# Performance work log

Measured on AMD Instinct MI355X. Metric: run time of the kernel, lower is better.

## Reference

```python
import jax, jax.numpy as jnp
from jax import lax
import numpy as np

IMG = 1024
STRIDES = (4, 8, 16, 32, 64)
FEAT_HW = (256, 128, 64, 32, 16)
ANCHOR_SCALE = 8.0          # per-level scale multiplier of stride
RATIOS = (0.5, 1.0, 2.0)
N_ANCHOR = len(RATIOS)
PRE_NMS = 6000
POST_NMS = 300
NMS_THRESH = 0.7
MIN_SIZE = 16.0
IMG_SCALE = 1.0
NEG = -1e9


def _conv(x, w, b, pad):
    y = lax.conv_general_dilated(x, w, (1, 1), [(pad, pad), (pad, pad)],
                                 dimension_numbers=("NCHW", "OIHW", "NCHW"))
    return y + b[None, :, None, None]


def _level_anchors(H, W, stride):
    # base anchors (ymin,xmin,ymax,xmax) centered at 0, one scale per level
    r = jnp.asarray(RATIOS, jnp.float32)
    hs = stride * ANCHOR_SCALE * jnp.sqrt(r)
    ws = stride * ANCHOR_SCALE * jnp.sqrt(1.0 / r)
    base = jnp.stack([-hs / 2, -ws / 2, hs / 2, ws / 2], axis=1)  # [A,4]
    ys = jnp.arange(H, dtype=jnp.float32) * stride
    xs = jnp.arange(W, dtype=jnp.float32) * stride
    gy, gx = jnp.meshgrid(ys, xs, indexing="ij")
    shift = jnp.stack([gy, gx, gy, gx], axis=-1).reshape(-1, 1, 4)   # [HW,1,4]
    return (shift + base[None, :, :]).reshape(-1, 4)                 # [HW*A,4]


def _decode(anchors, loc):
    ah = anchors[:, 2] - anchors[:, 0]
    aw = anchors[:, 3] - anchors[:, 1]
    acy = anchors[:, 0] + 0.5 * ah
    acx = anchors[:, 1] + 0.5 * aw
    dy, dx, dh, dw = loc[:, 0], loc[:, 1], loc[:, 2], loc[:, 3]
    cy = dy * ah + acy
    cx = dx * aw + acx
    h = jnp.exp(dh) * ah
    w = jnp.exp(dw) * aw
    boxes = jnp.stack([cy - 0.5 * h, cx - 0.5 * w, cy + 0.5 * h, cx + 0.5 * w], axis=1)
    return jnp.clip(boxes, 0.0, float(IMG))


def _iou_row(box, boxes):
    ty = jnp.maximum(box[0], boxes[:, 0])
    tx = jnp.maximum(box[1], boxes[:, 1])
    by = jnp.minimum(box[2], boxes[:, 2])
    bx = jnp.minimum(box[3], boxes[:, 3])
    inter = jnp.maximum(by - ty, 0.0) * jnp.maximum(bx - tx, 0.0)
    a1 = (box[2] - box[0]) * (box[3] - box[1])
    a2 = (boxes[:, 2] - boxes[:, 0]) * (boxes[:, 3] - boxes[:, 1])
    return inter / jnp.maximum(a1 + a2 - inter, 1e-9)


def _nms(boxes, scores):
    n = boxes.shape[0]
    idx_range = jnp.arange(n)

    def body(sc, _):
        i = jnp.argmax(sc)
        valid = sc[i] > NEG / 2
        iou = _iou_row(boxes[i], boxes)
        new_sc = jnp.where((iou > NMS_THRESH) | (idx_range == i), NEG, sc)
        sc = jnp.where(valid, new_sc, sc)
        return sc, (i, valid)

    _, (idx, keep) = lax.scan(body, scores, None, length=POST_NMS)
    return boxes[idx] * keep[:, None].astype(boxes.dtype)


def reference(p2, p3, p4, p5, p6, conv_w, conv_b, loc_w, loc_b, score_w, score_b):
    feats = [p2, p3, p4, p5, p6]
    locs, fgs, anchors = [], [], []
    for f, stride in zip(feats, STRIDES):
        h = jax.nn.relu(_conv(f, conv_w, conv_b, 1))
        loc = _conv(h, loc_w, loc_b, 0)        # [1,4A,H,W]
        sc = _conv(h, score_w, score_b, 0)     # [1,2A,H,W]
        H, W = loc.shape[2], loc.shape[3]
        loc = loc.transpose(0, 2, 3, 1).reshape(-1, 4)          # [HWA,4]
        sc = sc.transpose(0, 2, 3, 1).reshape(-1, 2)            # [HWA,2]
        fgs.append(jax.nn.softmax(sc, axis=-1)[:, 1])
        locs.append(loc)
        anchors.append(_level_anchors(H, W, stride))
    loc = jnp.concatenate(locs, axis=0)
    fg = jnp.concatenate(fgs, axis=0)
    anc = jnp.concatenate(anchors, axis=0)

    boxes = _decode(anc, loc)
    hh = boxes[:, 2] - boxes[:, 0]
    ww = boxes[:, 3] - boxes[:, 1]
    min_sz = MIN_SIZE * IMG_SCALE
    fg = jnp.where((hh >= min_sz) & (ww >= min_sz), fg, NEG)

    top_scores, top_idx = lax.top_k(fg, PRE_NMS)
    top_boxes = boxes[top_idx]
    rois = _nms(top_boxes, top_scores)   # [POST_NMS,4]
    return rois


def setup_inputs() -> dict:
    key = jax.random.key(0)
    ks = jax.random.split(key, 11)
    inp = {}
    for i, (name, hw) in enumerate(zip(["p2", "p3", "p4", "p5", "p6"], FEAT_HW)):
        inp[name] = jax.random.normal(ks[i], (1, 256, hw, hw), jnp.float32)
    inp["conv_w"] = 0.01 * jax.random.normal(ks[5], (256, 256, 3, 3), jnp.float32)
    inp["conv_b"] = jnp.zeros((256,), jnp.float32)
    inp["loc_w"] = 0.01 * jax.random.normal(ks[6], (12, 256, 1, 1), jnp.float32)
    inp["loc_b"] = jnp.zeros((12,), jnp.float32)
    inp["score_w"] = 0.01 * jax.random.normal(ks[7], (6, 256, 1, 1), jnp.float32)
    inp["score_b"] = jnp.zeros((6,), jnp.float32)
    return inp
```

## Files before the change

### kernel.cpp

```cpp
#include <hip/hip_runtime.h>
#include <hip/hip_bf16.h>

typedef unsigned int u32;
typedef unsigned long long u64;
typedef float v2f __attribute__((ext_vector_type(2)));

#define NEGV (-1000000000.0f)
#define N_ANCH 261888
#define PRE_NMS 6000
#define POST_NMS 300


__device__ __forceinline__ void gload_lds16(const float* g, float* l) {
    __builtin_amdgcn_global_load_lds((const __attribute__((address_space(1))) void*)g,
                                     (__attribute__((address_space(3))) void*)l, 16, 0, 0);
}

__device__ __forceinline__ int bucket_of(float s) {
    if (!(s > 0.0f)) return 0;
    float t = s * 4096.0f;
    int b = (int)t;
    return b > 4095 ? 4095 : b;
}

__global__ void kzero(u32* p) {
    for (int i = threadIdx.x; i < 4104; i += 1024) p[i] = 0u;
}

__global__ void wtrans(const float* __restrict__ cw, float* __restrict__ wt) {
    int g = blockIdx.x * 256 + threadIdx.x;
    int oc = g & 255; int cf = g >> 8;
    wt[g] = cw[oc * 2304 + cf];
}

__global__ __launch_bounds__(256, 6) void conv_head(
    const float* __restrict__ p2, const float* __restrict__ p3,
    const float* __restrict__ p4, const float* __restrict__ p5,
    const float* __restrict__ p6,
    const float* __restrict__ wt, const float* __restrict__ cb,
    const float* __restrict__ lw, const float* __restrict__ lb,
    const float* __restrict__ sw, const float* __restrict__ sb,
    float* __restrict__ scores_all, float4* __restrict__ boxes_all)
{
    __shared__ float smem[6656];
    float* Wl = smem;
    float* Il = smem + 4608;
    const int tid  = threadIdx.x;
    const int wv   = tid >> 6;
    const int lane = tid & 63;

    int bid = blockIdx.x;
    const float* in; int W, stride, abase, local, lgx;
    if (bid < 2048)      { in = p2; W = 256; stride = 4;  abase = 0;      local = bid;        lgx = 6; }
    else if (bid < 2560) { in = p3; W = 128; stride = 8;  abase = 196608; local = bid - 2048; lgx = 5; }
    else if (bid < 2688) { in = p4; W = 64;  stride = 16; abase = 245760; local = bid - 2560; lgx = 4; }
    else if (bid < 2720) { in = p5; W = 32;  stride = 32; abase = 258048; local = bid - 2688; lgx = 3; }
    else                 { in = p6; W = 16;  stride = 64; abase = 261120; local = bid - 2720; lgx = 2; }
    const int bx = local & ((1 << lgx) - 1), by = local >> lgx;
    const int gx0 = bx * 4, gy0 = by * 8;
    const int HW = W * W;

    v2f acc2[8][2];
#pragma unroll
    for (int i = 0; i < 8; ++i)
#pragma unroll
        for (int j = 0; j < 2; ++j) acc2[i][j] = (v2f){0.0f, 0.0f};

    const int icw = wv & 1, hw_ = wv >> 1;
    const int e = hw_ * 30 + lane;
    const int r0 = e / 6, c0 = e - r0 * 6;
    const int yg = gy0 - 1 + r0, xg = gx0 - 1 + c0;
    const bool act = (lane < 30);
    const bool inb = act && (yg >= 0 && yg < W && xg >= 0 && xg < W);
    const int iofs = yg * W + xg;

    for (int c = 0; c < 128; ++c) {
        __syncthreads();
        const float* gsrc = wt + c * 4608 + lane * 4;
#pragma unroll
        for (int k = 0; k < 5; ++k) {
            int row = wv + k * 4;
            if (row < 18) gload_lds16(gsrc + row * 256, Wl + row * 256);
        }
        const float* ibase = in + (size_t)(c * 2 + icw) * HW;
        if (act) {
            float v = inb ? ibase[iofs] : 0.0f;
            Il[icw * 80 + r0 * 8 + c0] = v;
        }
        __syncthreads();
#pragma unroll
        for (int ic = 0; ic < 2; ++ic) {
            float wk[9];
#pragma unroll
            for (int k = 0; k < 9; ++k) wk[k] = Wl[(ic * 9 + k) * 256 + tid];
#pragma unroll
            for (int iy = 0; iy < 10; ++iy) {
                float4 ra = *(const float4*)&Il[ic * 80 + iy * 8];
                float2 rc = *(const float2*)&Il[ic * 80 + iy * 8 + 4];
                float r6[6] = {ra.x, ra.y, ra.z, ra.w, rc.x, rc.y};
#pragma unroll
                for (int dy = 0; dy < 3; ++dy) {
                    const int ty = iy - dy;
                    if (ty >= 0 && ty < 8) {
                        const float w0 = wk[dy * 3 + 0], w1 = wk[dy * 3 + 1], w2 = wk[dy * 3 + 2];
#pragma unroll
                        for (int t = 0; t < 2; ++t) {
                            acc2[ty][t] = __builtin_elementwise_fma((v2f){w0, w0}, (v2f){r6[2*t+0], r6[2*t+1]}, acc2[ty][t]);
                            acc2[ty][t] = __builtin_elementwise_fma((v2f){w1, w1}, (v2f){r6[2*t+1], r6[2*t+2]}, acc2[ty][t]);
                            acc2[ty][t] = __builtin_elementwise_fma((v2f){w2, w2}, (v2f){r6[2*t+2], r6[2*t+3]}, acc2[ty][t]);
                        }
                    }
                }
            }
        }
    }
    {
        float bvv = cb[tid];
#pragma unroll
        for (int i = 0; i < 8; ++i)
#pragma unroll
            for (int j = 0; j < 2; ++j) {
                v2f t = acc2[i][j];
                t.x = fmaxf(t.x + bvv, 0.0f);
                t.y = fmaxf(t.y + bvv, 0.0f);
                acc2[i][j] = t;
            }
    }
    __syncthreads();
    float* hl = smem;
    float* ob = smem + 4160;

    for (int g = 0; g < 2; ++g) {
        __syncthreads();
#pragma unroll
        for (int p = 0; p < 16; ++p) {
            const int ty = (g << 2) + (p >> 2), tx = p & 3;
            hl[p * 260 + tid] = acc2[ty][tx >> 1][tx & 1];
        }
        __syncthreads();
        for (int it = tid; it < 288; it += 256) {
            int px = it / 18, o = it - px * 18;
            float a = (o < 12) ? lb[o] : sb[o - 12];
            const float* wrow = (o < 12) ? (lw + o * 256) : (sw + (o - 12) * 256);
            const float4* hv4 = (const float4*)&hl[px * 260];
            const float4* wv4 = (const float4*)wrow;
#pragma unroll 8
            for (int cc = 0; cc < 64; ++cc) {
                float4 hv = hv4[cc], wq = wv4[cc];
                a += hv.x * wq.x; a += hv.y * wq.y; a += hv.z * wq.z; a += hv.w * wq.w;
            }
            ob[px * 20 + o] = a;
        }
        __syncthreads();
        if (tid < 48) {
            int px = tid / 3, a = tid - px * 3;
            int gy = gy0 + (g << 2) + (px >> 2);
            int gx = gx0 + (px & 3);
            float dy = ob[px * 20 + a * 4 + 0];
            float dx = ob[px * 20 + a * 4 + 1];
            float dh = ob[px * 20 + a * 4 + 2];
            float dw = ob[px * 20 + a * 4 + 3];
            float s0 = ob[px * 20 + 12 + a * 2];
            float s1 = ob[px * 20 + 13 + a * 2];
            float mm = fmaxf(s0, s1);
            float e0 = expf(s0 - mm), e1x = expf(s1 - mm);
            float fg = e1x / (e0 + e1x);
            float sqa = (a == 0) ? 0.70710678f : ((a == 1) ? 1.0f : 1.41421356f);
            float sqb = (a == 0) ? 1.41421356f : ((a == 1) ? 1.0f : 0.70710678f);
            float s8 = (float)(stride * 8);
            float hs = __fmul_rn(s8, sqa), wsz = __fmul_rn(s8, sqb);
            float g_y = (float)(gy * stride), g_x = (float)(gx * stride);
            float a_y1 = __fsub_rn(g_y, __fmul_rn(hs, 0.5f));
            float a_y2 = __fadd_rn(g_y, __fmul_rn(hs, 0.5f));
            float a_x1 = __fsub_rn(g_x, __fmul_rn(wsz, 0.5f));
            float a_x2 = __fadd_rn(g_x, __fmul_rn(wsz, 0.5f));
            float ah = __fsub_rn(a_y2, a_y1), aw = __fsub_rn(a_x2, a_x1);
            float acy = __fadd_rn(a_y1, __fmul_rn(0.5f, ah));
            float acx = __fadd_rn(a_x1, __fmul_rn(0.5f, aw));
            float cy = __fadd_rn(__fmul_rn(dy, ah), acy);
            float cx = __fadd_rn(__fmul_rn(dx, aw), acx);
            float bh = __fmul_rn(expf(dh), ah);
            float bw = __fmul_rn(expf(dw), aw);
            float y1 = __fsub_rn(cy, __fmul_rn(0.5f, bh));
            float x1 = __fsub_rn(cx, __fmul_rn(0.5f, bw));
            float y2 = __fadd_rn(cy, __fmul_rn(0.5f, bh));
            float x2 = __fadd_rn(cx, __fmul_rn(0.5f, bw));
            y1 = fminf(fmaxf(y1, 0.0f), 1024.0f); x1 = fminf(fmaxf(x1, 0.0f), 1024.0f);
            y2 = fminf(fmaxf(y2, 0.0f), 1024.0f); x2 = fminf(fmaxf(x2, 0.0f), 1024.0f);
            float hh2 = __fsub_rn(y2, y1), ww2 = __fsub_rn(x2, x1);
            float sc = (hh2 >= 16.0f && ww2 >= 16.0f) ? fg : NEGV;
            int A = abase + (gy * W + gx) * 3 + a;
            scores_all[A] = sc;
            boxes_all[A] = make_float4(y1, x1, y2, x2);
        }
    }
}

__global__ void hist_k(const float* __restrict__ scores, u32* __restrict__ hist) {
    __shared__ u32 h[4096];
    int tid = threadIdx.x;
    for (int i = tid; i < 4096; i += 256) h[i] = 0u;
    __syncthreads();
    int gid = blockIdx.x * 256 + tid;
    int gs = gridDim.x * 256;
    for (int i = gid; i < N_ANCH; i += gs)
        atomicAdd(&h[bucket_of(scores[i])], 1u);
    __syncthreads();
    for (int i = tid; i < 4096; i += 256) if (h[i]) atomicAdd(&hist[i], h[i]);
}

__global__ void select_bucket(const u32* __restrict__ hist, u32* __restrict__ cnts) {
    int lane = threadIdx.x;
    u32 S = 0;
    for (int c = 0; c < 64; ++c) {
        int bin = 4095 - (c * 64 + lane);
        u32 cnt = hist[bin];
        u32 cum = cnt;
        for (int off = 1; off < 64; off <<= 1) {
            u32 n = __shfl_up(cum, off, 64);
            if (lane >= off) cum += n;
        }
        u64 ball = __ballot(S + cum >= (u32)PRE_NMS);
        if (ball) {
            int l = __ffsll((long long)ball) - 1;
            if (lane == 0) cnts[2] = (u32)(4095 - (c * 64 + l));
            return;
        }
        S += __shfl(cum, 63, 64);
    }
    if (lane == 0) cnts[2] = 0u;
}

__global__ void compact_k(const float* __restrict__ scores, u32* __restrict__ cnts,
                          u64* __restrict__ cand) {
    int B = (int)cnts[2];
    int gid = blockIdx.x * blockDim.x + threadIdx.x;
    int gs = gridDim.x * blockDim.x;
    for (int i = gid; i < N_ANCH; i += gs) {
        float s = scores[i];
        if (bucket_of(s) >= B) {
            u32 pos = atomicAdd(&cnts[0], 1u);
            if (pos < 8192u) {
                u32 u = __float_as_uint(s);
                u32 key = (u & 0x80000000u) ? ~u : (u | 0x80000000u);
                cand[pos] = ((u64)key << 32) | (u64)((u32)(~i));
            }
        }
    }
}

__global__ __launch_bounds__(1024) void sort_gather(
    const u64* __restrict__ cand, const u32* __restrict__ cnts,
    const float* __restrict__ sall, const float4* __restrict__ ball,
    float* __restrict__ nsc, float4* __restrict__ nbx, u32* __restrict__ nvalid)
{
    __shared__ u64 srt[8192];
    int tid = threadIdx.x;
    u32 total = cnts[0]; if (total > 8192u) total = 8192u;
    for (int i = tid; i < 8192; i += 1024) srt[i] = (i < (int)total) ? cand[i] : 0ULL;
    __syncthreads();
    for (int k = 2; k <= 8192; k <<= 1) {
        for (int j = k >> 1; j > 0; j >>= 1) {
            for (int i = tid; i < 8192; i += 1024) {
                int l = i ^ j;
                if (l > i) {
                    u64 a = srt[i], b = srt[l];
                    bool descRegion = (i & k) == 0;
                    if (descRegion ? (a < b) : (a > b)) { srt[i] = b; srt[l] = a; }
                }
            }
            __syncthreads();
        }
    }
    int local = 0;
    for (int i = tid; i < PRE_NMS; i += 1024) {
        u64 comp = srt[i];
        u32 idx = ~((u32)(comp & 0xFFFFFFFFULL));
        float s; float4 bx;
        if (idx < (u32)N_ANCH) { s = sall[idx]; bx = ball[idx]; }
        else { s = NEGV; bx = make_float4(0.f, 0.f, 0.f, 0.f); }
        nsc[i] = s;
        nbx[i] = bx;
        if (s > -5.0e8f) local++;
    }
    for (int off = 32; off > 0; off >>= 1) local += __shfl_down(local, off, 64);
    if ((tid & 63) == 0) atomicAdd(nvalid, (u32)local);
}

__global__ void ioumat(const float4* __restrict__ bxs, u64* __restrict__ mat) {
    int i = blockIdx.x;
    int w = threadIdx.x;
    if (w >= 94) return;
    float4 bi = bxs[i];
    float a1 = (bi.z - bi.x) * (bi.w - bi.y);
    u64 bits = 0ULL;
    int j0 = w * 64;
    for (int b = 0; b < 64; ++b) {
        int j = j0 + b;
        if (j < PRE_NMS) {
            float4 bj = bxs[j];
            float ty = fmaxf(bi.x, bj.x), tx = fmaxf(bi.y, bj.y);
            float by = fminf(bi.z, bj.z), bx = fminf(bi.w, bj.w);
            float inter = fmaxf(by - ty, 0.0f) * fmaxf(bx - tx, 0.0f);
            float a2 = (bj.z - bj.x) * (bj.w - bj.y);
            float iou = inter / fmaxf(a1 + a2 - inter, 1e-9f);
            if (iou > 0.7f) bits |= (1ULL << b);
        }
    }
    mat[(size_t)i * 94 + w] = bits;
}

__global__ void greedy(const u64* __restrict__ mat, const float* __restrict__ nbxf,
                       const u32* __restrict__ nvalid, float* __restrict__ out) {
    int lane = threadIdx.x;
    u64 rem0 = 0ULL, rem1 = 0ULL;
    int nv = (int)*nvalid; if (nv > PRE_NMS) nv = PRE_NMS;
    int kept = 0;
    for (int widx = 0; widx * 64 < nv && kept < POST_NMS; ++widx) {
        u64 word = (widx < 64) ? __shfl(rem0, widx, 64) : __shfl(rem1, widx - 64, 64);
        int bmax = nv - widx * 64; if (bmax > 64) bmax = 64;
        for (int b = 0; b < bmax; ++b) {
            if (!((word >> b) & 1ULL)) {
                int i = widx * 64 + b;
                const u64* row = mat + (size_t)i * 94;
                rem0 |= row[lane];
                if (lane < 30) rem1 |= row[64 + lane];
                if (lane < 4) out[kept * 4 + lane] = nbxf[i * 4 + lane];
                ++kept;
                if (kept == POST_NMS) break;
                word = (widx < 64) ? __shfl(rem0, widx, 64) : __shfl(rem1, widx - 64, 64);
            }
        }
        if (kept == POST_NMS) break;
    }
    for (int idx = kept * 4 + lane; idx < POST_NMS * 4; idx += 64) out[idx] = 0.0f;
}

extern "C" void kernel_launch(void* const* d_in, const int* in_sizes, int n_in,
                              void* d_out, int out_size, void* d_ws, size_t ws_size,
                              hipStream_t stream) {
    const float* p2 = (const float*)d_in[0];
    const float* p3 = (const float*)d_in[1];
    const float* p4 = (const float*)d_in[2];
    const float* p5 = (const float*)d_in[3];
    const float* p6 = (const float*)d_in[4];
    const float* cw = (const float*)d_in[5];
    const float* cb = (const float*)d_in[6];
    const float* lw = (const float*)d_in[7];
    const float* lb = (const float*)d_in[8];
    const float* sw = (const float*)d_in[9];
    const float* sb = (const float*)d_in[10];
    float* out = (float*)d_out;
    char* ws = (char*)d_ws;

    float*  scores_all = (float*)(ws + 0);
    float4* boxes_all  = (float4*)(ws + 0x100000);
    u32*    hist       = (u32*)(ws + 0x500000);
    u32*    cnts       = (u32*)(ws + 0x504000);
    u64*    cand       = (u64*)(ws + 0x505000);
    float*  nsc        = (float*)(ws + 0x520000);
    float4* nbx        = (float4*)(ws + 0x526000);
    u64*    mat        = (u64*)(ws + 0x540000);
    float*  wt         = (float*)(ws + 0x540000);

    hipLaunchKernelGGL(kzero, dim3(1), dim3(1024), 0, stream, hist);
    hipLaunchKernelGGL(wtrans, dim3(2304), dim3(256), 0, stream, cw, wt);
    hipLaunchKernelGGL(conv_head, dim3(2728), dim3(256), 0, stream,
                       p2, p3, p4, p5, p6, wt, cb, lw, lb, sw, sb,
                       scores_all, boxes_all);
    hipLaunchKernelGGL(hist_k, dim3(64), dim3(256), 0, stream, scores_all, hist);
    hipLaunchKernelGGL(select_bucket, dim3(1), dim3(64), 0, stream, hist, cnts);
    hipLaunchKernelGGL(compact_k, dim3(512), dim3(256), 0, stream, scores_all, cnts, cand);
    hipLaunchKernelGGL(sort_gather, dim3(1), dim3(1024), 0, stream,
                       cand, cnts, scores_all, boxes_all, nsc, nbx, cnts + 1);
    hipLaunchKernelGGL(ioumat, dim3(PRE_NMS), dim3(128), 0, stream, nbx, mat);
    hipLaunchKernelGGL(greedy, dim3(1), dim3(64), 0, stream, mat, (const float*)nbx, cnts + 1, out);
}
```

Before: 1.999 ms.

## Pack row pairs into v2f lanes for conv and fold hist zeroing into wtrans

The 3x3 conv inner loop is restructured so each v2f accumulator lane holds pixels from rows y and y+4, rather than adjacent x pixels. Each staged input element is then a packed pair, so every packed FMA uses one LDS-loaded v2f directly with a splatted weight. This removes the per-iteration repacking of unaligned scalar pairs and reduces the LDS reads per FMA. Separately, the kzero launch is removed and histogram zeroing is folded into the wtrans kernel, saving one kernel launch. The output-writing index mapping is adjusted to match the new accumulator layout.

```diff
diff --git a/kernel.cpp b/kernel.cpp
--- a/kernel.cpp
+++ b/kernel.cpp
@@ -4,6 +4,7 @@
 typedef unsigned int u32;
 typedef unsigned long long u64;
 typedef float v2f __attribute__((ext_vector_type(2)));
+typedef float v4f __attribute__((ext_vector_type(4)));
 
 #define NEGV (-1000000000.0f)
 #define N_ANCH 261888
@@ -23,14 +24,11 @@
     return b > 4095 ? 4095 : b;
 }
 
-__global__ void kzero(u32* p) {
-    for (int i = threadIdx.x; i < 4104; i += 1024) p[i] = 0u;
-}
-
-__global__ void wtrans(const float* __restrict__ cw, float* __restrict__ wt) {
+__global__ void wtrans(const float* __restrict__ cw, float* __restrict__ wt, u32* __restrict__ hist) {
     int g = blockIdx.x * 256 + threadIdx.x;
     int oc = g & 255; int cf = g >> 8;
     wt[g] = cw[oc * 2304 + cf];
+    if (g < 4104) hist[g] = 0u;
 }
 
 __global__ __launch_bounds__(256, 6) void conv_head(
@@ -44,7 +42,7 @@
 {
     __shared__ float smem[6656];
     float* Wl = smem;
-    float* Il = smem + 4608;
+    v2f*   IpL = (v2f*)(smem + 4608);
     const int tid  = threadIdx.x;
     const int wv   = tid >> 6;
     const int lane = tid & 63;
@@ -60,19 +58,22 @@
     const int gx0 = bx * 4, gy0 = by * 8;
     const int HW = W * W;
 
-    v2f acc2[8][2];
-#pragma unroll
-    for (int i = 0; i < 8; ++i)
-#pragma unroll
-        for (int j = 0; j < 2; ++j) acc2[i][j] = (v2f){0.0f, 0.0f};
-
-    const int icw = wv & 1, hw_ = wv >> 1;
-    const int e = hw_ * 30 + lane;
-    const int r0 = e / 6, c0 = e - r0 * 6;
-    const int yg = gy0 - 1 + r0, xg = gx0 - 1 + c0;
-    const bool act = (lane < 30);
-    const bool inb = act && (yg >= 0 && yg < W && xg >= 0 && xg < W);
-    const int iofs = yg * W + xg;
+    v2f acc2[4][4];
+#pragma unroll
+    for (int i = 0; i < 4; ++i)
+#pragma unroll
+        for (int j = 0; j < 4; ++j) acc2[i][j] = (v2f){0.0f, 0.0f};
+
+    const int icw = wv & 1, halfw = wv >> 1;
+    const int ee = halfw * 18 + lane;
+    const int iy = ee / 6, xx = ee - iy * 6;
+    const int ylo = gy0 - 1 + iy, yhi = ylo + 4, xg = gx0 - 1 + xx;
+    const bool act = (lane < 18);
+    const bool aLo = act && (ylo >= 0 && ylo < W && xg >= 0 && xg < W);
+    const bool aHi = act && (yhi >= 0 && yhi < W && xg >= 0 && xg < W);
+    const int ofsLo = ylo * W + xg;
+    const int ofsHi = yhi * W + xg;
+    const int ipidx = (icw * 6 + iy) * 8 + xx;
 
     for (int c = 0; c < 128; ++c) {
         __syncthreads();
@@ -84,31 +85,39 @@
         }
         const float* ibase = in + (size_t)(c * 2 + icw) * HW;
         if (act) {
-            float v = inb ? ibase[iofs] : 0.0f;
-            Il[icw * 80 + r0 * 8 + c0] = v;
+            float vlo = aLo ? ibase[ofsLo] : 0.0f;
+            float vhi = aHi ? ibase[ofsHi] : 0.0f;
+            IpL[ipidx] = (v2f){vlo, vhi};
         }
         __syncthreads();
 #pragma unroll
         for (int ic = 0; ic < 2; ++ic) {
-            float wk[9];
-#pragma unroll
-            for (int k = 0; k < 9; ++k) wk[k] = Wl[(ic * 9 + k) * 256 + tid];
-#pragma unroll
-            for (int iy = 0; iy < 10; ++iy) {
-                float4 ra = *(const float4*)&Il[ic * 80 + iy * 8];
-                float2 rc = *(const float2*)&Il[ic * 80 + iy * 8 + 4];
-                float r6[6] = {ra.x, ra.y, ra.z, ra.w, rc.x, rc.y};
+            v2f wk2[9];
+#pragma unroll
+            for (int k = 0; k < 9; ++k) {
+                float w_ = Wl[(ic * 9 + k) * 256 + tid];
+                wk2[k] = (v2f){w_, w_};
+            }
+#pragma unroll
+            for (int ip = 0; ip < 6; ++ip) {
+                const v4f* rq = (const v4f*)&IpL[(ic * 6 + ip) * 8];
+                v4f q0 = rq[0], q1 = rq[1], q2 = rq[2];
+                v2f iw[6];
+                iw[0] = __builtin_shufflevector(q0, q0, 0, 1);
+                iw[1] = __builtin_shufflevector(q0, q0, 2, 3);
+                iw[2] = __builtin_shufflevector(q1, q1, 0, 1);
+                iw[3] = __builtin_shufflevector(q1, q1, 2, 3);
+                iw[4] = __builtin_shufflevector(q2, q2, 0, 1);
+                iw[5] = __builtin_shufflevector(q2, q2, 2, 3);
 #pragma unroll
                 for (int dy = 0; dy < 3; ++dy) {
-                    const int ty = iy - dy;
-                    if (ty >= 0 && ty < 8) {
-                        const float w0 = wk[dy * 3 + 0], w1 = wk[dy * 3 + 1], w2 = wk[dy * 3 + 2];
-#pragma unroll
-                        for (int t = 0; t < 2; ++t) {
-                            acc2[ty][t] = __builtin_elementwise_fma((v2f){w0, w0}, (v2f){r6[2*t+0], r6[2*t+1]}, acc2[ty][t]);
-                            acc2[ty][t] = __builtin_elementwise_fma((v2f){w1, w1}, (v2f){r6[2*t+1], r6[2*t+2]}, acc2[ty][t]);
-                            acc2[ty][t] = __builtin_elementwise_fma((v2f){w2, w2}, (v2f){r6[2*t+2], r6[2*t+3]}, acc2[ty][t]);
-                        }
+                    const int tp = ip - dy;
+                    if (tp >= 0 && tp < 4) {
+#pragma unroll
+                        for (int tx = 0; tx < 4; ++tx)
+#pragma unroll
+                            for (int dx = 0; dx < 3; ++dx)
+                                acc2[tp][tx] = __builtin_elementwise_fma(wk2[dy * 3 + dx], iw[tx + dx], acc2[tp][tx]);
                     }
                 }
             }
@@ -117,9 +126,9 @@
     {
         float bvv = cb[tid];
 #pragma unroll
-        for (int i = 0; i < 8; ++i)
-#pragma unroll
-            for (int j = 0; j < 2; ++j) {
+        for (int i = 0; i < 4; ++i)
+#pragma unroll
+            for (int j = 0; j < 4; ++j) {
                 v2f t = acc2[i][j];
                 t.x = fmaxf(t.x + bvv, 0.0f);
                 t.y = fmaxf(t.y + bvv, 0.0f);
@@ -134,8 +143,8 @@
         __syncthreads();
 #pragma unroll
         for (int p = 0; p < 16; ++p) {
-            const int ty = (g << 2) + (p >> 2), tx = p & 3;
-            hl[p * 260 + tid] = acc2[ty][tx >> 1][tx & 1];
+            const int pr = p >> 2, tx = p & 3;
+            hl[p * 260 + tid] = g ? acc2[pr][tx].y : acc2[pr][tx].x;
         }
         __syncthreads();
         for (int it = tid; it < 288; it += 256) {
@@ -363,8 +372,7 @@
     u64*    mat        = (u64*)(ws + 0x540000);
     float*  wt         = (float*)(ws + 0x540000);
 
-    hipLaunchKernelGGL(kzero, dim3(1), dim3(1024), 0, stream, hist);
-    hipLaunchKernelGGL(wtrans, dim3(2304), dim3(256), 0, stream, cw, wt);
+    hipLaunchKernelGGL(wtrans, dim3(2304), dim3(256), 0, stream, cw, wt, hist);
     hipLaunchKernelGGL(conv_head, dim3(2728), dim3(256), 0, stream,
                        p2, p3, p4, p5, p6, wt, cb, lw, lb, sw, sb,
                        scores_all, boxes_all);
```

After: 1.940 ms. -3.0%, faster.
